# Kernel tuning notes

Hardware: AMD Instinct MI355X
Metric: run time of the kernel (lower is better)

The kernel has to match this reference:

```python
import jax, jax.numpy as jnp
import numpy as np

LEAK = 0.01  # torch LeakyReLU default negative_slope

def lrelu(x):
    return jnp.where(x >= 0, x, LEAK * x)

def edge_conv(x, src, dst, ea, W1, b1, W2, b2):
    # message: cat(x_i=target, x_j=source, edge_attr) -> Linear -> LeakyReLU -> Linear
    m = jnp.concatenate([x[dst], x[src], ea], axis=1)          # [E, 2F+Fe]
    h = lrelu(m @ W1 + b1) @ W2 + b2                            # [E, H]
    n = x.shape[0]
    agg = jnp.full((n, h.shape[1]), jnp.inf, h.dtype).at[dst].min(h)  # scatter-min at target
    return jnp.where(jnp.isfinite(agg), agg, jnp.zeros_like(agg))     # empty nodes -> 0


def setup_inputs() -> dict:
    key = jax.random.key(0)
    ks = jax.random.split(key, 20)
    B, N, E = 4, 20000, 640000
    NF, AD, EF, H = 2, 1, 1, 8
    inp = {
        "node_features": jax.random.randint(ks[0], (B, N, NF), 0, 10, dtype=jnp.int32),
        "actions": jax.random.normal(ks[1], (B, N), dtype=jnp.float32),
        "edge_index": jax.random.randint(ks[2], (B, 2, E), 0, N, dtype=jnp.int64),
        "edge_features": jax.random.normal(ks[3], (B, E, EF), dtype=jnp.float32),
    }
    d0 = NF + AD  # 3
    def lin(k, fin, fout):
        s = 1.0 / np.sqrt(fin)
        k1, k2 = jax.random.split(k)
        return (jax.random.uniform(k1, (fin, fout), jnp.float32, -s, s),
                jax.random.uniform(k2, (fout,), jnp.float32, -s, s))
    inp["c1_W1"], inp["c1_b1"] = lin(ks[4], 2 * d0 + EF, H)
    inp["c1_W2"], inp["c1_b2"] = lin(ks[5], H, H)
    inp["c2_W1"], inp["c2_b1"] = lin(ks[6], 2 * H + 1, H)
    inp["c2_W2"], inp["c2_b2"] = lin(ks[7], H, H)
    inp["c3_W1"], inp["c3_b1"] = lin(ks[8], 2 * H + 1, H)
    inp["c3_W2"], inp["c3_b2"] = lin(ks[9], H, H)
    inp["lin_W"], inp["lin_b"] = lin(ks[10], d0 + H, 1)
    return inp


def reference(node_features, actions, edge_index, edge_features,
              c1_W1, c1_b1, c1_W2, c1_b2,
              c2_W1, c2_b1, c2_W2, c2_b2,
              c3_W1, c3_b1, c3_W2, c3_b2,
              lin_W, lin_b):
    # x = int(node_features) concat actions  -> float
    x0 = jnp.concatenate([node_features.astype(jnp.int32).astype(jnp.float32),
                          actions[..., None]], axis=-1)  # [B,N,3]

    def per_graph(x0g, eig, eag):
        src, dst = eig[0], eig[1]  # flow source_to_target: x_j=src, x_i=dst
        h = lrelu(edge_conv(x0g, src, dst, eag, c1_W1, c1_b1, c1_W2, c1_b2))
        h = lrelu(edge_conv(h, src, dst, eag, c2_W1, c2_b1, c2_W2, c2_b2))
        h = lrelu(edge_conv(h, src, dst, eag, c3_W1, c3_b1, c3_W2, c3_b2))
        xc = jnp.concatenate([x0g, h], axis=1)  # [N, 3+8]
        return jnp.sum(xc, axis=0)              # sum-pool over nodes

    pooled = jax.vmap(per_graph)(x0, edge_index, edge_features)  # [B, 11]
    return pooled @ lin_W + lin_b  # [B, 1]
```

## Files before the change

### kernel.cpp

```cpp
#include <hip/hip_runtime.h>

#define LEAK 0.01f
#define BS 128
#define PCHUNK 8192
#define MAXTB 2048

__device__ __forceinline__ float lrelu(float v) {
    return v >= 0.f ? v : LEAK * v;
}

__device__ __forceinline__ unsigned int fmin_encode(float x) {
    unsigned int u = __float_as_uint(x);
    return (u & 0x80000000u) ? ~u : (u | 0x80000000u);
}
__device__ __forceinline__ float fmin_decode(unsigned int k) {
    unsigned int u = (k & 0x80000000u) ? (k ^ 0x80000000u) : ~k;
    return __uint_as_float(u);
}


__global__ __launch_bounds__(256) void node_init_kernel(
    const int* __restrict__ nf, const float* __restrict__ act,
    float* __restrict__ x0, int BN) {
    int tid = blockIdx.x * blockDim.x + threadIdx.x;
    if (tid >= BN) return;
    x0[tid * 3 + 0] = (float)nf[tid * 2 + 0];
    x0[tid * 3 + 1] = (float)nf[tid * 2 + 1];
    x0[tid * 3 + 2] = act[tid];
}

__global__ __launch_bounds__(256) void pool_kernel(
    const float* __restrict__ x0, const float* __restrict__ h,
    const float* __restrict__ lw, const float* __restrict__ lb,
    float* __restrict__ out, int N) {
    int b = blockIdx.y;
    int n = blockIdx.x * blockDim.x + threadIdx.x;
    float c = 0.f;
    if (n < N) {
        const float* x = x0 + ((size_t)b * N + n) * 3;
        const float* hh = h + ((size_t)b * N + n) * 8;
        c = x[0] * lw[0] + x[1] * lw[1] + x[2] * lw[2];
#pragma unroll
        for (int k = 0; k < 8; ++k) c = fmaf(hh[k], lw[3 + k], c);
    }
#pragma unroll
    for (int off = 32; off > 0; off >>= 1) c += __shfl_down(c, off, 64);
    __shared__ float wsum[4];
    int lane = threadIdx.x & 63;
    int wave = threadIdx.x >> 6;
    if (lane == 0) wsum[wave] = c;
    __syncthreads();
    if (threadIdx.x == 0) {
        float s = wsum[0] + wsum[1] + wsum[2] + wsum[3];
        if (blockIdx.x == 0) s += lb[0];
        atomicAdd(&out[b], s);
    }
}

template <int D>
__global__ __launch_bounds__(256) void precompute_kernel(
    const float* __restrict__ x, const float* __restrict__ W1,
    const float* __restrict__ b1, float* __restrict__ a1,
    float* __restrict__ a2, int BN) {
    int i = blockIdx.x * blockDim.x + threadIdx.x;
    if (i >= BN) return;
    float xi[D];
#pragma unroll
    for (int k = 0; k < D; ++k) xi[k] = x[(size_t)i * D + k];
    float v1[8], v2[8];
#pragma unroll
    for (int j = 0; j < 8; ++j) { v1[j] = b1[j]; v2[j] = 0.f; }
#pragma unroll
    for (int k = 0; k < D; ++k) {
        float xk = xi[k];
#pragma unroll
        for (int j = 0; j < 8; ++j) {
            v1[j] = fmaf(xk, W1[k * 8 + j], v1[j]);
            v2[j] = fmaf(xk, W1[(D + k) * 8 + j], v2[j]);
        }
    }
    float4* o1 = (float4*)(a1 + (size_t)i * 8);
    float4* o2 = (float4*)(a2 + (size_t)i * 8);
    o1[0] = make_float4(v1[0], v1[1], v1[2], v1[3]);
    o1[1] = make_float4(v1[4], v1[5], v1[6], v1[7]);
    o2[0] = make_float4(v2[0], v2[1], v2[2], v2[3]);
    o2[1] = make_float4(v2[4], v2[5], v2[6], v2[7]);
}


__global__ __launch_bounds__(256) void bucket_hist_kernel(
    const int* __restrict__ ei, int* __restrict__ bcnt,
    int E, int NB, int TB, int BE) {
    __shared__ int lc[MAXTB];
    int t = threadIdx.x;
    for (int i = t; i < TB; i += 256) lc[i] = 0;
    __syncthreads();
    int start = blockIdx.x * PCHUNK;
    int end = min(start + PCHUNK, BE);
    for (int e = start + t; e < end; e += 256) {
        int b = e / E;
        int idx = e - b * E;
        int d = ei[(size_t)b * 2 * E + E + idx];
        atomicAdd(&lc[b * NB + (d >> 7)], 1);
    }
    __syncthreads();
    for (int i = t; i < TB; i += 256)
        if (lc[i]) atomicAdd(&bcnt[i], lc[i]);
}

__global__ __launch_bounds__(1024) void bucket_scan_kernel(
    const int* __restrict__ bcnt, int* __restrict__ base,
    int* __restrict__ fill, int TB) {
    __shared__ int ts[1024];
    int t = threadIdx.x;
    int i0 = 2 * t, i1 = 2 * t + 1;
    int v0 = (i0 < TB) ? bcnt[i0] : 0;
    int v1 = (i1 < TB) ? bcnt[i1] : 0;
    int s = v0 + v1;
    ts[t] = s;
    __syncthreads();
    int incl = s;
    for (int off = 1; off < 1024; off <<= 1) {
        int add = (t >= off) ? ts[t - off] : 0;
        __syncthreads();
        incl += add;
        ts[t] = incl;
        __syncthreads();
    }
    int ex = incl - s;
    if (i0 < TB) { base[i0] = ex; fill[i0] = ex; }
    if (i1 < TB) { base[i1] = ex + v0; fill[i1] = ex + v0; }
    if (t == 0) base[TB] = ts[1023];
}

__global__ __launch_bounds__(256) void part_kernel(
    const int* __restrict__ ei, const float* __restrict__ ea,
    int* __restrict__ fill, int2* __restrict__ pairs,
    int E, int NB, int TB, int BE) {
    __shared__ int lc[MAXTB];
    __shared__ int lbase[MAXTB];
    int t = threadIdx.x;
    for (int i = t; i < TB; i += 256) lc[i] = 0;
    __syncthreads();
    int start = blockIdx.x * PCHUNK;
    int pk[32];
    for (int j = 0; j < 32; ++j) {
        int e = start + j * 256 + t;
        int p = -1;
        if (e < BE) {
            int b = e / E;
            int idx = e - b * E;
            int d = ei[(size_t)b * 2 * E + E + idx];
            int bkt = b * NB + (d >> 7);
            int r = atomicAdd(&lc[bkt], 1);
            p = bkt | (r << 12);
        }
        pk[j] = p;
    }
    __syncthreads();
    for (int i = t; i < TB; i += 256) {
        int c = lc[i];
        lbase[i] = c ? atomicAdd(&fill[i], c) : 0;
    }
    __syncthreads();
    for (int j = 0; j < 32; ++j) {
        int e = start + j * 256 + t;
        if (e < BE) {
            int b = e / E;
            int idx = e - b * E;
            const int* eb = ei + (size_t)b * 2 * E;
            int s = eb[idx];
            int d = eb[E + idx];
            int bkt = pk[j] & 0xFFF;
            int r = pk[j] >> 12;
            int pos = lbase[bkt] + r;
            pairs[pos] = make_int2(s | ((d & 127) << 16), __float_as_int(ea[e]));
        }
    }
}


__global__ __launch_bounds__(256) void conv_bucket_kernel(
    const float* __restrict__ a1, const float* __restrict__ a2,
    const float* __restrict__ w1e, const float* __restrict__ W2,
    const float* __restrict__ b2, const int* __restrict__ base,
    const int2* __restrict__ pairs, float* __restrict__ hout,
    int N, int NB) {
    __shared__ float a1s[BS * 9];
    __shared__ unsigned int acc[BS * 9];
    int bkt = blockIdx.x;
    int b = bkt / NB;
    int n0 = (bkt - b * NB) << 7;
    int nCnt = min(BS, N - n0);
    int t = threadIdx.x;
    size_t gn0 = ((size_t)b * N + n0) * 8;

    for (int i = t; i < nCnt * 8; i += 256)
        a1s[(i >> 3) * 9 + (i & 7)] = a1[gn0 + i];
    for (int i = t; i < BS * 9; i += 256) acc[i] = 0xFFFFFFFFu;

    float we[8], bb[8];
#pragma unroll
    for (int j = 0; j < 8; ++j) { we[j] = w1e[j]; bb[j] = b2[j]; }
    __syncthreads();

    int k1 = base[bkt + 1];
    size_t a2base = (size_t)b * N * 8;
    for (int k = base[bkt] + t; k < k1; k += 256) {
        int2 p = pairs[k];
        int s = p.x & 0xFFFF;
        int dl = (p.x >> 16) & 127;
        float eav = __int_as_float(p.y);
        const float4* a2p = (const float4*)(a2 + a2base + (size_t)s * 8);
        float4 lo = a2p[0], hi = a2p[1];
        float h1[8];
        h1[0] = a1s[dl * 9 + 0] + lo.x; h1[1] = a1s[dl * 9 + 1] + lo.y;
        h1[2] = a1s[dl * 9 + 2] + lo.z; h1[3] = a1s[dl * 9 + 3] + lo.w;
        h1[4] = a1s[dl * 9 + 4] + hi.x; h1[5] = a1s[dl * 9 + 5] + hi.y;
        h1[6] = a1s[dl * 9 + 6] + hi.z; h1[7] = a1s[dl * 9 + 7] + hi.w;
#pragma unroll
        for (int j = 0; j < 8; ++j) {
            h1[j] = fmaf(eav, we[j], h1[j]);
            h1[j] = lrelu(h1[j]);
        }
        float h2[8];
#pragma unroll
        for (int j = 0; j < 8; ++j) h2[j] = bb[j];
#pragma unroll
        for (int kk = 0; kk < 8; ++kk) {
            float hk = h1[kk];
#pragma unroll
            for (int j = 0; j < 8; ++j) h2[j] = fmaf(hk, W2[kk * 8 + j], h2[j]);
        }
#pragma unroll
        for (int j = 0; j < 8; ++j)
            atomicMin(&acc[dl * 9 + j], fmin_encode(h2[j]));
    }
    __syncthreads();

    for (int i = t; i < nCnt * 8; i += 256) {
        float v = fmin_decode(acc[(i >> 3) * 9 + (i & 7)]);
        unsigned int u = __float_as_uint(v);
        if ((u & 0x7F800000u) == 0x7F800000u) v = 0.f;
        hout[gn0 + i] = lrelu(v);
    }
}


template <int D>
__global__ __launch_bounds__(256) void edge_conv_kernel(
    const float* __restrict__ x, const int* __restrict__ ei,
    const float* __restrict__ ea,
    const float* __restrict__ W1, const float* __restrict__ b1,
    const float* __restrict__ W2, const float* __restrict__ b2,
    unsigned int* __restrict__ agg, int E, int N, int B) {
    int tid = blockIdx.x * blockDim.x + threadIdx.x;
    if (tid >= B * E) return;
    int b = tid / E;
    int e = tid - b * E;
    const int* eb = ei + (size_t)b * 2 * E;
    int s = eb[e];
    int d = eb[E + e];
    const float* xi = x + ((size_t)b * N + d) * D;
    const float* xj = x + ((size_t)b * N + s) * D;
    constexpr int M = 2 * D + 1;
    float m[M];
#pragma unroll
    for (int k = 0; k < D; ++k) { m[k] = xi[k]; m[D + k] = xj[k]; }
    m[2 * D] = ea[(size_t)b * E + e];
    float h1[8];
#pragma unroll
    for (int j = 0; j < 8; ++j) h1[j] = b1[j];
#pragma unroll
    for (int k = 0; k < M; ++k) {
        float mk = m[k];
#pragma unroll
        for (int j = 0; j < 8; ++j) h1[j] = fmaf(mk, W1[k * 8 + j], h1[j]);
    }
#pragma unroll
    for (int j = 0; j < 8; ++j) h1[j] = lrelu(h1[j]);
    float h2[8];
#pragma unroll
    for (int j = 0; j < 8; ++j) h2[j] = b2[j];
#pragma unroll
    for (int k = 0; k < 8; ++k) {
        float hk = h1[k];
#pragma unroll
        for (int j = 0; j < 8; ++j) h2[j] = fmaf(hk, W2[k * 8 + j], h2[j]);
    }
    unsigned int* ag = agg + ((size_t)b * N + d) * 8;
#pragma unroll
    for (int j = 0; j < 8; ++j) atomicMin(&ag[j], fmin_encode(h2[j]));
}

__global__ __launch_bounds__(256) void finalize_kernel(
    unsigned int* __restrict__ agg, int total) {
    int tid = blockIdx.x * blockDim.x + threadIdx.x;
    if (tid >= total) return;
    float v = fmin_decode(agg[tid]);
    unsigned int u = __float_as_uint(v);
    if ((u & 0x7F800000u) == 0x7F800000u) v = 0.f;
    ((float*)agg)[tid] = lrelu(v);
}


static inline size_t align256(size_t x) { return (x + 255) & ~(size_t)255; }

extern "C" void kernel_launch(void* const* d_in, const int* in_sizes, int n_in,
                              void* d_out, int out_size, void* d_ws, size_t ws_size,
                              hipStream_t stream) {
    const int B = 4;
    const int N = in_sizes[1] / B;
    const int E = in_sizes[2] / (2 * B);

    const int*   nf  = (const int*)d_in[0];
    const float* act = (const float*)d_in[1];
    const int*   ei  = (const int*)d_in[2];
    const float* ea  = (const float*)d_in[3];
    const float* c1_W1 = (const float*)d_in[4];
    const float* c1_b1 = (const float*)d_in[5];
    const float* c1_W2 = (const float*)d_in[6];
    const float* c1_b2 = (const float*)d_in[7];
    const float* c2_W1 = (const float*)d_in[8];
    const float* c2_b1 = (const float*)d_in[9];
    const float* c2_W2 = (const float*)d_in[10];
    const float* c2_b2 = (const float*)d_in[11];
    const float* c3_W1 = (const float*)d_in[12];
    const float* c3_b1 = (const float*)d_in[13];
    const float* c3_W2 = (const float*)d_in[14];
    const float* c3_b2 = (const float*)d_in[15];
    const float* lw    = (const float*)d_in[16];
    const float* lb    = (const float*)d_in[17];
    float* out = (float*)d_out;

    const int BN = B * N;
    const int BE = B * E;
    const int NB = (N + BS - 1) / BS;
    const int TB = B * NB;

    char* ws = (char*)d_ws;
    size_t off = 0;
    float* x0   = (float*)(ws + off);  off += align256((size_t)BN * 3 * 4);
    float* bufA = (float*)(ws + off);  off += align256((size_t)BN * 8 * 4);
    float* bufB = (float*)(ws + off);  off += align256((size_t)BN * 8 * 4);
    float* a1   = (float*)(ws + off);  off += align256((size_t)BN * 8 * 4);
    float* a2   = (float*)(ws + off);  off += align256((size_t)BN * 8 * 4);
    int* bcnt   = (int*)(ws + off);    off += align256((size_t)TB * 4);
    int* base   = (int*)(ws + off);    off += align256((size_t)(TB + 1) * 4);
    int* fill   = (int*)(ws + off);    off += align256((size_t)TB * 4);
    int2* pairs = (int2*)(ws + off);   off += align256((size_t)BE * 8);
    const bool useFast = (off <= ws_size) && (TB <= MAXTB) && (N <= 65536);

    hipMemsetAsync(out, 0, (size_t)B * sizeof(float), stream);
    node_init_kernel<<<(BN + 255) / 256, 256, 0, stream>>>(nf, act, x0, BN);

    const int ngrid = (BN + 255) / 256;
    const int pgrid1 = (BE + PCHUNK - 1) / PCHUNK;

    if (useFast) {
        hipMemsetAsync(bcnt, 0, (size_t)TB * 4, stream);
        bucket_hist_kernel<<<pgrid1, 256, 0, stream>>>(ei, bcnt, E, NB, TB, BE);
        bucket_scan_kernel<<<1, 1024, 0, stream>>>(bcnt, base, fill, TB);
        part_kernel<<<pgrid1, 256, 0, stream>>>(ei, ea, fill, pairs, E, NB, TB, BE);

        precompute_kernel<3><<<ngrid, 256, 0, stream>>>(x0, c1_W1, c1_b1, a1, a2, BN);
        conv_bucket_kernel<<<TB, 256, 0, stream>>>(a1, a2, c1_W1 + 6 * 8, c1_W2, c1_b2,
                                                   base, pairs, bufA, N, NB);
        precompute_kernel<8><<<ngrid, 256, 0, stream>>>(bufA, c2_W1, c2_b1, a1, a2, BN);
        conv_bucket_kernel<<<TB, 256, 0, stream>>>(a1, a2, c2_W1 + 16 * 8, c2_W2, c2_b2,
                                                   base, pairs, bufB, N, NB);
        precompute_kernel<8><<<ngrid, 256, 0, stream>>>(bufB, c3_W1, c3_b1, a1, a2, BN);
        conv_bucket_kernel<<<TB, 256, 0, stream>>>(a1, a2, c3_W1 + 16 * 8, c3_W2, c3_b2,
                                                   base, pairs, bufA, N, NB);
    } else {
        const int egrid = (BE + 255) / 256;
        const int aggTotal = BN * 8;
        const int agrid = (aggTotal + 255) / 256;
        const size_t aggBytes = (size_t)aggTotal * 4;
        unsigned int* uA = (unsigned int*)bufA;
        unsigned int* uB = (unsigned int*)bufB;

        hipMemsetAsync(uA, 0xFF, aggBytes, stream);
        edge_conv_kernel<3><<<egrid, 256, 0, stream>>>(
            x0, ei, ea, c1_W1, c1_b1, c1_W2, c1_b2, uA, E, N, B);
        finalize_kernel<<<agrid, 256, 0, stream>>>(uA, aggTotal);

        hipMemsetAsync(uB, 0xFF, aggBytes, stream);
        edge_conv_kernel<8><<<egrid, 256, 0, stream>>>(
            (const float*)uA, ei, ea, c2_W1, c2_b1, c2_W2, c2_b2, uB, E, N, B);
        finalize_kernel<<<agrid, 256, 0, stream>>>(uB, aggTotal);

        hipMemsetAsync(uA, 0xFF, aggBytes, stream);
        edge_conv_kernel<8><<<egrid, 256, 0, stream>>>(
            (const float*)uB, ei, ea, c3_W1, c3_b1, c3_W2, c3_b2, uA, E, N, B);
        finalize_kernel<<<agrid, 256, 0, stream>>>(uA, aggTotal);
    }

    dim3 pgrid((N + 255) / 256, B);
    pool_kernel<<<pgrid, 256, 0, stream>>>(x0, (const float*)bufA, lw, lb, out, N);
}
```

Measured before the change: 247.1 us.

## Fuse node init, next-layer precompute and pooling into bucketed conv kernels

The fast path now does node init, first-layer precompute and the x0 part of pooling in one kernel. Each conv layer's epilogue computes the next layer's a1/a2 projections from shared memory, and the last conv pools directly into the output. This removes the separate precompute, pool and init launches along with their global round-trips. It also partitions edges per graph with a 2D grid and smaller chunks, avoiding the per-edge division, and processes two edges per thread iteration to raise memory-level parallelism. The cost is more work in the conv epilogues and a larger partition grid with more global atomics.

```diff
diff --git a/kernel.cpp b/kernel.cpp
--- a/kernel.cpp
+++ b/kernel.cpp
@@ -2,8 +2,8 @@
 
 #define LEAK 0.01f
 #define BS 128
-#define PCHUNK 8192
-#define MAXTB 2048
+#define PCHUNK 2048
+#define MAXNB 1024
 
 __device__ __forceinline__ float lrelu(float v) {
     return v >= 0.f ? v : LEAK * v;
@@ -16,6 +16,285 @@
 __device__ __forceinline__ float fmin_decode(unsigned int k) {
     unsigned int u = (k & 0x80000000u) ? (k ^ 0x80000000u) : ~k;
     return __uint_as_float(u);
+}
+
+__device__ __forceinline__ void block_add(float c, float* dst) {
+    __shared__ float wsum[4];
+#pragma unroll
+    for (int off = 32; off > 0; off >>= 1) c += __shfl_down(c, off, 64);
+    int lane = threadIdx.x & 63;
+    int wave = threadIdx.x >> 6;
+    if (lane == 0) wsum[wave] = c;
+    __syncthreads();
+    if (threadIdx.x == 0)
+        atomicAdd(dst, wsum[0] + wsum[1] + wsum[2] + wsum[3]);
+}
+
+__global__ __launch_bounds__(256) void init_pre1_kernel(
+    const int* __restrict__ nf, const float* __restrict__ act,
+    const float* __restrict__ W1, const float* __restrict__ b1,
+    const float* __restrict__ lw, const float* __restrict__ lb,
+    float* __restrict__ a1, float* __restrict__ a2,
+    float* __restrict__ out, int N) {
+    int b = blockIdx.y;
+    int n = blockIdx.x * 256 + threadIdx.x;
+    float c = 0.f;
+    if (n < N) {
+        size_t i = (size_t)b * N + n;
+        float x0 = (float)nf[i * 2 + 0];
+        float x1 = (float)nf[i * 2 + 1];
+        float x2 = act[i];
+        float v1[8], v2[8];
+#pragma unroll
+        for (int j = 0; j < 8; ++j) {
+            v1[j] = b1[j] + x0 * W1[0 * 8 + j] + x1 * W1[1 * 8 + j] + x2 * W1[2 * 8 + j];
+            v2[j] =         x0 * W1[3 * 8 + j] + x1 * W1[4 * 8 + j] + x2 * W1[5 * 8 + j];
+        }
+        float4* o1 = (float4*)(a1 + i * 8);
+        float4* o2 = (float4*)(a2 + i * 8);
+        o1[0] = make_float4(v1[0], v1[1], v1[2], v1[3]);
+        o1[1] = make_float4(v1[4], v1[5], v1[6], v1[7]);
+        o2[0] = make_float4(v2[0], v2[1], v2[2], v2[3]);
+        o2[1] = make_float4(v2[4], v2[5], v2[6], v2[7]);
+        c = x0 * lw[0] + x1 * lw[1] + x2 * lw[2];
+        if (n == 0) c += lb[0];
+    }
+    block_add(c, &out[b]);
+}
+
+
+__global__ __launch_bounds__(256) void bucket_hist_kernel(
+    const int* __restrict__ ei, int* __restrict__ bcnt, int E, int NB) {
+    __shared__ int lc[MAXNB];
+    int b = blockIdx.y;
+    int t = threadIdx.x;
+    for (int i = t; i < NB; i += 256) lc[i] = 0;
+    __syncthreads();
+    int e0 = blockIdx.x * PCHUNK;
+    int end = min(e0 + PCHUNK, E);
+    const int* drow = ei + (size_t)b * 2 * E + E;
+    for (int e = e0 + t; e < end; e += 256)
+        atomicAdd(&lc[drow[e] >> 7], 1);
+    __syncthreads();
+    for (int i = t; i < NB; i += 256)
+        if (lc[i]) atomicAdd(&bcnt[b * NB + i], lc[i]);
+}
+
+__global__ __launch_bounds__(1024) void bucket_scan_kernel(
+    const int* __restrict__ bcnt, int* __restrict__ base,
+    int* __restrict__ fill, int TB) {
+    __shared__ int ts[1024];
+    int t = threadIdx.x;
+    int i0 = 2 * t, i1 = 2 * t + 1;
+    int v0 = (i0 < TB) ? bcnt[i0] : 0;
+    int v1 = (i1 < TB) ? bcnt[i1] : 0;
+    int s = v0 + v1;
+    ts[t] = s;
+    __syncthreads();
+    int incl = s;
+    for (int off = 1; off < 1024; off <<= 1) {
+        int add = (t >= off) ? ts[t - off] : 0;
+        __syncthreads();
+        incl += add;
+        ts[t] = incl;
+        __syncthreads();
+    }
+    int ex = incl - s;
+    if (i0 < TB) { base[i0] = ex; fill[i0] = ex; }
+    if (i1 < TB) { base[i1] = ex + v0; fill[i1] = ex + v0; }
+    if (t == 0) base[TB] = ts[1023];
+}
+
+__global__ __launch_bounds__(256) void part_kernel(
+    const int* __restrict__ ei, const float* __restrict__ ea,
+    int* __restrict__ fill, int2* __restrict__ pairs, int E, int NB) {
+    __shared__ int lc[MAXNB];
+    __shared__ int lbase[MAXNB];
+    int b = blockIdx.y;
+    int t = threadIdx.x;
+    for (int i = t; i < NB; i += 256) lc[i] = 0;
+    __syncthreads();
+    int e0 = blockIdx.x * PCHUNK;
+    int end = min(e0 + PCHUNK, E);
+    const int* srow = ei + (size_t)b * 2 * E;
+    const int* drow = srow + E;
+    int pk[PCHUNK / 256];
+#pragma unroll
+    for (int j = 0; j < PCHUNK / 256; ++j) {
+        int e = e0 + j * 256 + t;
+        int p = -1;
+        if (e < end) {
+            int d = drow[e];
+            int bin = d >> 7;
+            int r = atomicAdd(&lc[bin], 1);
+            p = bin | ((d & 127) << 10) | (r << 17);
+        }
+        pk[j] = p;
+    }
+    __syncthreads();
+    for (int i = t; i < NB; i += 256) {
+        int c = lc[i];
+        lbase[i] = c ? atomicAdd(&fill[b * NB + i], c) : 0;
+    }
+    __syncthreads();
+#pragma unroll
+    for (int j = 0; j < PCHUNK / 256; ++j) {
+        int e = e0 + j * 256 + t;
+        if (e < end) {
+            int p = pk[j];
+            int bin = p & 1023;
+            int dl = (p >> 10) & 127;
+            int r = p >> 17;
+            pairs[lbase[bin] + r] =
+                make_int2(srow[e] | (dl << 16), __float_as_int(ea[(size_t)b * E + e]));
+        }
+    }
+}
+
+
+__device__ __forceinline__ void conv_edges(
+    const float* __restrict__ a2g, const float* we, const float* bb,
+    const float* __restrict__ W2, const int2* __restrict__ pairs,
+    int k0, int k1, const float* __restrict__ a1s, unsigned int* __restrict__ acc) {
+    int t = threadIdx.x;
+    for (int k = k0 + t; k < k1; k += 512) {
+        int2 p0 = pairs[k];
+        bool has1 = (k + 256 < k1);
+        int2 p1 = has1 ? pairs[k + 256] : p0;
+        const float4* q0 = (const float4*)(a2g + (size_t)(p0.x & 0xFFFF) * 8);
+        float4 lo0 = q0[0], hi0 = q0[1];
+        const float4* q1 = (const float4*)(a2g + (size_t)(p1.x & 0xFFFF) * 8);
+        float4 lo1 = q1[0], hi1 = q1[1];
+#pragma unroll
+        for (int which = 0; which < 2; ++which) {
+            if (which == 1 && !has1) break;
+            int dl = ((which ? p1.x : p0.x) >> 16) & 127;
+            float eav = __int_as_float(which ? p1.y : p0.y);
+            float4 lo = which ? lo1 : lo0;
+            float4 hi = which ? hi1 : hi0;
+            float h1[8];
+            h1[0] = a1s[dl * 9 + 0] + lo.x; h1[1] = a1s[dl * 9 + 1] + lo.y;
+            h1[2] = a1s[dl * 9 + 2] + lo.z; h1[3] = a1s[dl * 9 + 3] + lo.w;
+            h1[4] = a1s[dl * 9 + 4] + hi.x; h1[5] = a1s[dl * 9 + 5] + hi.y;
+            h1[6] = a1s[dl * 9 + 6] + hi.z; h1[7] = a1s[dl * 9 + 7] + hi.w;
+#pragma unroll
+            for (int j = 0; j < 8; ++j) {
+                h1[j] = fmaf(eav, we[j], h1[j]);
+                h1[j] = lrelu(h1[j]);
+            }
+            float h2[8];
+#pragma unroll
+            for (int j = 0; j < 8; ++j) h2[j] = bb[j];
+#pragma unroll
+            for (int kk = 0; kk < 8; ++kk) {
+                float hk = h1[kk];
+#pragma unroll
+                for (int j = 0; j < 8; ++j) h2[j] = fmaf(hk, W2[kk * 8 + j], h2[j]);
+            }
+#pragma unroll
+            for (int j = 0; j < 8; ++j)
+                atomicMin(&acc[dl * 9 + j], fmin_encode(h2[j]));
+        }
+    }
+}
+
+__global__ __launch_bounds__(256) void conv_mid_kernel(
+    const float* __restrict__ a1, const float* __restrict__ a2,
+    const float* __restrict__ w1e, const float* __restrict__ W2,
+    const float* __restrict__ b2,
+    const float* __restrict__ nW1, const float* __restrict__ nb1,
+    const int* __restrict__ base, const int2* __restrict__ pairs,
+    float* __restrict__ na1, float* __restrict__ na2, int N, int NB) {
+    __shared__ float a1s[BS * 9];
+    __shared__ unsigned int acc[BS * 9];
+    int b = blockIdx.y;
+    int bkt = b * NB + blockIdx.x;
+    int n0 = blockIdx.x << 7;
+    int nCnt = min(BS, N - n0);
+    int t = threadIdx.x;
+    size_t gn0 = ((size_t)b * N + n0) * 8;
+
+    for (int i = t; i < nCnt * 8; i += 256)
+        a1s[(i >> 3) * 9 + (i & 7)] = a1[gn0 + i];
+    for (int i = t; i < BS * 9; i += 256) acc[i] = 0xFFFFFFFFu;
+    float we[8], bb[8];
+#pragma unroll
+    for (int j = 0; j < 8; ++j) { we[j] = w1e[j]; bb[j] = b2[j]; }
+    __syncthreads();
+
+    conv_edges(a2 + (size_t)b * N * 8, we, bb, W2, pairs, base[bkt], base[bkt + 1],
+               a1s, acc);
+    __syncthreads();
+
+    for (int i = t; i < nCnt * 8; i += 256) {
+        float v = fmin_decode(acc[(i >> 3) * 9 + (i & 7)]);
+        unsigned int u = __float_as_uint(v);
+        if ((u & 0x7F800000u) == 0x7F800000u) v = 0.f;
+        a1s[(i >> 3) * 9 + (i & 7)] = lrelu(v);
+    }
+    __syncthreads();
+
+    int node = t >> 1, half = t & 1;
+    if (node < nCnt) {
+        float h[8];
+#pragma unroll
+        for (int j = 0; j < 8; ++j) h[j] = a1s[node * 9 + j];
+        float v[8];
+#pragma unroll
+        for (int j = 0; j < 8; ++j) v[j] = half ? 0.f : nb1[j];
+        const float* Wbase = nW1 + (half ? 64 : 0);
+#pragma unroll
+        for (int k = 0; k < 8; ++k) {
+            float hk = h[k];
+#pragma unroll
+            for (int j = 0; j < 8; ++j) v[j] = fmaf(hk, Wbase[k * 8 + j], v[j]);
+        }
+        float* dst = (half ? na2 : na1) + gn0 + (size_t)node * 8;
+        float4* o = (float4*)dst;
+        o[0] = make_float4(v[0], v[1], v[2], v[3]);
+        o[1] = make_float4(v[4], v[5], v[6], v[7]);
+    }
+}
+
+__global__ __launch_bounds__(256) void conv_final_kernel(
+    const float* __restrict__ a1, const float* __restrict__ a2,
+    const float* __restrict__ w1e, const float* __restrict__ W2,
+    const float* __restrict__ b2, const float* __restrict__ lw,
+    const int* __restrict__ base, const int2* __restrict__ pairs,
+    float* __restrict__ out, int N, int NB) {
+    __shared__ float a1s[BS * 9];
+    __shared__ unsigned int acc[BS * 9];
+    int b = blockIdx.y;
+    int bkt = b * NB + blockIdx.x;
+    int n0 = blockIdx.x << 7;
+    int nCnt = min(BS, N - n0);
+    int t = threadIdx.x;
+    size_t gn0 = ((size_t)b * N + n0) * 8;
+
+    for (int i = t; i < nCnt * 8; i += 256)
+        a1s[(i >> 3) * 9 + (i & 7)] = a1[gn0 + i];
+    for (int i = t; i < BS * 9; i += 256) acc[i] = 0xFFFFFFFFu;
+    float we[8], bb[8];
+#pragma unroll
+    for (int j = 0; j < 8; ++j) { we[j] = w1e[j]; bb[j] = b2[j]; }
+    __syncthreads();
+
+    conv_edges(a2 + (size_t)b * N * 8, we, bb, W2, pairs, base[bkt], base[bkt + 1],
+               a1s, acc);
+    __syncthreads();
+
+    float c = 0.f;
+    if (t < nCnt) {
+#pragma unroll
+        for (int j = 0; j < 8; ++j) {
+            float v = fmin_decode(acc[t * 9 + j]);
+            unsigned int u = __float_as_uint(v);
+            if ((u & 0x7F800000u) == 0x7F800000u) v = 0.f;
+            c = fmaf(lrelu(v), lw[3 + j], c);
+        }
+    }
+    __syncthreads();
+    block_add(c, &out[b]);
 }
 
 
@@ -28,224 +307,6 @@
     x0[tid * 3 + 1] = (float)nf[tid * 2 + 1];
     x0[tid * 3 + 2] = act[tid];
 }
-
-__global__ __launch_bounds__(256) void pool_kernel(
-    const float* __restrict__ x0, const float* __restrict__ h,
-    const float* __restrict__ lw, const float* __restrict__ lb,
-    float* __restrict__ out, int N) {
-    int b = blockIdx.y;
-    int n = blockIdx.x * blockDim.x + threadIdx.x;
-    float c = 0.f;
-    if (n < N) {
-        const float* x = x0 + ((size_t)b * N + n) * 3;
-        const float* hh = h + ((size_t)b * N + n) * 8;
-        c = x[0] * lw[0] + x[1] * lw[1] + x[2] * lw[2];
-#pragma unroll
-        for (int k = 0; k < 8; ++k) c = fmaf(hh[k], lw[3 + k], c);
-    }
-#pragma unroll
-    for (int off = 32; off > 0; off >>= 1) c += __shfl_down(c, off, 64);
-    __shared__ float wsum[4];
-    int lane = threadIdx.x & 63;
-    int wave = threadIdx.x >> 6;
-    if (lane == 0) wsum[wave] = c;
-    __syncthreads();
-    if (threadIdx.x == 0) {
-        float s = wsum[0] + wsum[1] + wsum[2] + wsum[3];
-        if (blockIdx.x == 0) s += lb[0];
-        atomicAdd(&out[b], s);
-    }
-}
-
-template <int D>
-__global__ __launch_bounds__(256) void precompute_kernel(
-    const float* __restrict__ x, const float* __restrict__ W1,
-    const float* __restrict__ b1, float* __restrict__ a1,
-    float* __restrict__ a2, int BN) {
-    int i = blockIdx.x * blockDim.x + threadIdx.x;
-    if (i >= BN) return;
-    float xi[D];
-#pragma unroll
-    for (int k = 0; k < D; ++k) xi[k] = x[(size_t)i * D + k];
-    float v1[8], v2[8];
-#pragma unroll
-    for (int j = 0; j < 8; ++j) { v1[j] = b1[j]; v2[j] = 0.f; }
-#pragma unroll
-    for (int k = 0; k < D; ++k) {
-        float xk = xi[k];
-#pragma unroll
-        for (int j = 0; j < 8; ++j) {
-            v1[j] = fmaf(xk, W1[k * 8 + j], v1[j]);
-            v2[j] = fmaf(xk, W1[(D + k) * 8 + j], v2[j]);
-        }
-    }
-    float4* o1 = (float4*)(a1 + (size_t)i * 8);
-    float4* o2 = (float4*)(a2 + (size_t)i * 8);
-    o1[0] = make_float4(v1[0], v1[1], v1[2], v1[3]);
-    o1[1] = make_float4(v1[4], v1[5], v1[6], v1[7]);
-    o2[0] = make_float4(v2[0], v2[1], v2[2], v2[3]);
-    o2[1] = make_float4(v2[4], v2[5], v2[6], v2[7]);
-}
-
-
-__global__ __launch_bounds__(256) void bucket_hist_kernel(
-    const int* __restrict__ ei, int* __restrict__ bcnt,
-    int E, int NB, int TB, int BE) {
-    __shared__ int lc[MAXTB];
-    int t = threadIdx.x;
-    for (int i = t; i < TB; i += 256) lc[i] = 0;
-    __syncthreads();
-    int start = blockIdx.x * PCHUNK;
-    int end = min(start + PCHUNK, BE);
-    for (int e = start + t; e < end; e += 256) {
-        int b = e / E;
-        int idx = e - b * E;
-        int d = ei[(size_t)b * 2 * E + E + idx];
-        atomicAdd(&lc[b * NB + (d >> 7)], 1);
-    }
-    __syncthreads();
-    for (int i = t; i < TB; i += 256)
-        if (lc[i]) atomicAdd(&bcnt[i], lc[i]);
-}
-
-__global__ __launch_bounds__(1024) void bucket_scan_kernel(
-    const int* __restrict__ bcnt, int* __restrict__ base,
-    int* __restrict__ fill, int TB) {
-    __shared__ int ts[1024];
-    int t = threadIdx.x;
-    int i0 = 2 * t, i1 = 2 * t + 1;
-    int v0 = (i0 < TB) ? bcnt[i0] : 0;
-    int v1 = (i1 < TB) ? bcnt[i1] : 0;
-    int s = v0 + v1;
-    ts[t] = s;
-    __syncthreads();
-    int incl = s;
-    for (int off = 1; off < 1024; off <<= 1) {
-        int add = (t >= off) ? ts[t - off] : 0;
-        __syncthreads();
-        incl += add;
-        ts[t] = incl;
-        __syncthreads();
-    }
-    int ex = incl - s;
-    if (i0 < TB) { base[i0] = ex; fill[i0] = ex; }
-    if (i1 < TB) { base[i1] = ex + v0; fill[i1] = ex + v0; }
-    if (t == 0) base[TB] = ts[1023];
-}
-
-__global__ __launch_bounds__(256) void part_kernel(
-    const int* __restrict__ ei, const float* __restrict__ ea,
-    int* __restrict__ fill, int2* __restrict__ pairs,
-    int E, int NB, int TB, int BE) {
-    __shared__ int lc[MAXTB];
-    __shared__ int lbase[MAXTB];
-    int t = threadIdx.x;
-    for (int i = t; i < TB; i += 256) lc[i] = 0;
-    __syncthreads();
-    int start = blockIdx.x * PCHUNK;
-    int pk[32];
-    for (int j = 0; j < 32; ++j) {
-        int e = start + j * 256 + t;
-        int p = -1;
-        if (e < BE) {
-            int b = e / E;
-            int idx = e - b * E;
-            int d = ei[(size_t)b * 2 * E + E + idx];
-            int bkt = b * NB + (d >> 7);
-            int r = atomicAdd(&lc[bkt], 1);
-            p = bkt | (r << 12);
-        }
-        pk[j] = p;
-    }
-    __syncthreads();
-    for (int i = t; i < TB; i += 256) {
-        int c = lc[i];
-        lbase[i] = c ? atomicAdd(&fill[i], c) : 0;
-    }
-    __syncthreads();
-    for (int j = 0; j < 32; ++j) {
-        int e = start + j * 256 + t;
-        if (e < BE) {
-            int b = e / E;
-            int idx = e - b * E;
-            const int* eb = ei + (size_t)b * 2 * E;
-            int s = eb[idx];
-            int d = eb[E + idx];
-            int bkt = pk[j] & 0xFFF;
-            int r = pk[j] >> 12;
-            int pos = lbase[bkt] + r;
-            pairs[pos] = make_int2(s | ((d & 127) << 16), __float_as_int(ea[e]));
-        }
-    }
-}
-
-
-__global__ __launch_bounds__(256) void conv_bucket_kernel(
-    const float* __restrict__ a1, const float* __restrict__ a2,
-    const float* __restrict__ w1e, const float* __restrict__ W2,
-    const float* __restrict__ b2, const int* __restrict__ base,
-    const int2* __restrict__ pairs, float* __restrict__ hout,
-    int N, int NB) {
-    __shared__ float a1s[BS * 9];
-    __shared__ unsigned int acc[BS * 9];
-    int bkt = blockIdx.x;
-    int b = bkt / NB;
-    int n0 = (bkt - b * NB) << 7;
-    int nCnt = min(BS, N - n0);
-    int t = threadIdx.x;
-    size_t gn0 = ((size_t)b * N + n0) * 8;
-
-    for (int i = t; i < nCnt * 8; i += 256)
-        a1s[(i >> 3) * 9 + (i & 7)] = a1[gn0 + i];
-    for (int i = t; i < BS * 9; i += 256) acc[i] = 0xFFFFFFFFu;
-
-    float we[8], bb[8];
-#pragma unroll
-    for (int j = 0; j < 8; ++j) { we[j] = w1e[j]; bb[j] = b2[j]; }
-    __syncthreads();
-
-    int k1 = base[bkt + 1];
-    size_t a2base = (size_t)b * N * 8;
-    for (int k = base[bkt] + t; k < k1; k += 256) {
-        int2 p = pairs[k];
-        int s = p.x & 0xFFFF;
-        int dl = (p.x >> 16) & 127;
-        float eav = __int_as_float(p.y);
-        const float4* a2p = (const float4*)(a2 + a2base + (size_t)s * 8);
-        float4 lo = a2p[0], hi = a2p[1];
-        float h1[8];
-        h1[0] = a1s[dl * 9 + 0] + lo.x; h1[1] = a1s[dl * 9 + 1] + lo.y;
-        h1[2] = a1s[dl * 9 + 2] + lo.z; h1[3] = a1s[dl * 9 + 3] + lo.w;
-        h1[4] = a1s[dl * 9 + 4] + hi.x; h1[5] = a1s[dl * 9 + 5] + hi.y;
-        h1[6] = a1s[dl * 9 + 6] + hi.z; h1[7] = a1s[dl * 9 + 7] + hi.w;
-#pragma unroll
-        for (int j = 0; j < 8; ++j) {
-            h1[j] = fmaf(eav, we[j], h1[j]);
-            h1[j] = lrelu(h1[j]);
-        }
-        float h2[8];
-#pragma unroll
-        for (int j = 0; j < 8; ++j) h2[j] = bb[j];
-#pragma unroll
-        for (int kk = 0; kk < 8; ++kk) {
-            float hk = h1[kk];
-#pragma unroll
-            for (int j = 0; j < 8; ++j) h2[j] = fmaf(hk, W2[kk * 8 + j], h2[j]);
-        }
-#pragma unroll
-        for (int j = 0; j < 8; ++j)
-            atomicMin(&acc[dl * 9 + j], fmin_encode(h2[j]));
-    }
-    __syncthreads();
-
-    for (int i = t; i < nCnt * 8; i += 256) {
-        float v = fmin_decode(acc[(i >> 3) * 9 + (i & 7)]);
-        unsigned int u = __float_as_uint(v);
-        if ((u & 0x7F800000u) == 0x7F800000u) v = 0.f;
-        hout[gn0 + i] = lrelu(v);
-    }
-}
-
 
 template <int D>
 __global__ __launch_bounds__(256) void edge_conv_kernel(
@@ -301,6 +362,24 @@
     unsigned int u = __float_as_uint(v);
     if ((u & 0x7F800000u) == 0x7F800000u) v = 0.f;
     ((float*)agg)[tid] = lrelu(v);
+}
+
+__global__ __launch_bounds__(256) void pool_kernel(
+    const float* __restrict__ x0, const float* __restrict__ h,
+    const float* __restrict__ lw, const float* __restrict__ lb,
+    float* __restrict__ out, int N) {
+    int b = blockIdx.y;
+    int n = blockIdx.x * blockDim.x + threadIdx.x;
+    float c = 0.f;
+    if (n < N) {
+        const float* x = x0 + ((size_t)b * N + n) * 3;
+        const float* hh = h + ((size_t)b * N + n) * 8;
+        c = x[0] * lw[0] + x[1] * lw[1] + x[2] * lw[2];
+#pragma unroll
+        for (int k = 0; k < 8; ++k) c = fmaf(hh[k], lw[3 + k], c);
+        if (n == 0) c += lb[0];
+    }
+    block_add(c, &out[b]);
 }
 
 
@@ -337,48 +416,54 @@
     const int BE = B * E;
     const int NB = (N + BS - 1) / BS;
     const int TB = B * NB;
+    const int CPG = (E + PCHUNK - 1) / PCHUNK;
 
     char* ws = (char*)d_ws;
     size_t off = 0;
-    float* x0   = (float*)(ws + off);  off += align256((size_t)BN * 3 * 4);
-    float* bufA = (float*)(ws + off);  off += align256((size_t)BN * 8 * 4);
-    float* bufB = (float*)(ws + off);  off += align256((size_t)BN * 8 * 4);
-    float* a1   = (float*)(ws + off);  off += align256((size_t)BN * 8 * 4);
-    float* a2   = (float*)(ws + off);  off += align256((size_t)BN * 8 * 4);
+    float* a1A  = (float*)(ws + off);  off += align256((size_t)BN * 8 * 4);
+    float* a2A  = (float*)(ws + off);  off += align256((size_t)BN * 8 * 4);
+    float* a1B  = (float*)(ws + off);  off += align256((size_t)BN * 8 * 4);
+    float* a2B  = (float*)(ws + off);  off += align256((size_t)BN * 8 * 4);
     int* bcnt   = (int*)(ws + off);    off += align256((size_t)TB * 4);
     int* base   = (int*)(ws + off);    off += align256((size_t)(TB + 1) * 4);
     int* fill   = (int*)(ws + off);    off += align256((size_t)TB * 4);
     int2* pairs = (int2*)(ws + off);   off += align256((size_t)BE * 8);
-    const bool useFast = (off <= ws_size) && (TB <= MAXTB) && (N <= 65536);
+    float* x0   = (float*)(ws + off);  off += align256((size_t)BN * 3 * 4);
+    const bool useFast = (off <= ws_size) && (NB <= MAXNB) && (TB <= 2048) &&
+                         (N <= 65536);
 
     hipMemsetAsync(out, 0, (size_t)B * sizeof(float), stream);
-    node_init_kernel<<<(BN + 255) / 256, 256, 0, stream>>>(nf, act, x0, BN);
-
-    const int ngrid = (BN + 255) / 256;
-    const int pgrid1 = (BE + PCHUNK - 1) / PCHUNK;
 
     if (useFast) {
+        dim3 egrid(CPG, B);
+        dim3 igrid((N + 255) / 256, B);
+        dim3 cgrid(NB, B);
+
         hipMemsetAsync(bcnt, 0, (size_t)TB * 4, stream);
-        bucket_hist_kernel<<<pgrid1, 256, 0, stream>>>(ei, bcnt, E, NB, TB, BE);
+        init_pre1_kernel<<<igrid, 256, 0, stream>>>(nf, act, c1_W1, c1_b1,
+                                                    lw, lb, a1A, a2A, out, N);
+        bucket_hist_kernel<<<egrid, 256, 0, stream>>>(ei, bcnt, E, NB);
         bucket_scan_kernel<<<1, 1024, 0, stream>>>(bcnt, base, fill, TB);
-        part_kernel<<<pgrid1, 256, 0, stream>>>(ei, ea, fill, pairs, E, NB, TB, BE);
-
-        precompute_kernel<3><<<ngrid, 256, 0, stream>>>(x0, c1_W1, c1_b1, a1, a2, BN);
-        conv_bucket_kernel<<<TB, 256, 0, stream>>>(a1, a2, c1_W1 + 6 * 8, c1_W2, c1_b2,
-                                                   base, pairs, bufA, N, NB);
-        precompute_kernel<8><<<ngrid, 256, 0, stream>>>(bufA, c2_W1, c2_b1, a1, a2, BN);
-        conv_bucket_kernel<<<TB, 256, 0, stream>>>(a1, a2, c2_W1 + 16 * 8, c2_W2, c2_b2,
-                                                   base, pairs, bufB, N, NB);
-        precompute_kernel<8><<<ngrid, 256, 0, stream>>>(bufB, c3_W1, c3_b1, a1, a2, BN);
-        conv_bucket_kernel<<<TB, 256, 0, stream>>>(a1, a2, c3_W1 + 16 * 8, c3_W2, c3_b2,
-                                                   base, pairs, bufA, N, NB);
+        part_kernel<<<egrid, 256, 0, stream>>>(ei, ea, fill, pairs, E, NB);
+
+        conv_mid_kernel<<<cgrid, 256, 0, stream>>>(
+            a1A, a2A, c1_W1 + 6 * 8, c1_W2, c1_b2, c2_W1, c2_b1,
+            base, pairs, a1B, a2B, N, NB);
+        conv_mid_kernel<<<cgrid, 256, 0, stream>>>(
+            a1B, a2B, c2_W1 + 16 * 8, c2_W2, c2_b2, c3_W1, c3_b1,
+            base, pairs, a1A, a2A, N, NB);
+        conv_final_kernel<<<cgrid, 256, 0, stream>>>(
+            a1A, a2A, c3_W1 + 16 * 8, c3_W2, c3_b2, lw,
+            base, pairs, out, N, NB);
     } else {
         const int egrid = (BE + 255) / 256;
         const int aggTotal = BN * 8;
         const int agrid = (aggTotal + 255) / 256;
         const size_t aggBytes = (size_t)aggTotal * 4;
-        unsigned int* uA = (unsigned int*)bufA;
-        unsigned int* uB = (unsigned int*)bufB;
+        unsigned int* uA = (unsigned int*)a1A;
+        unsigned int* uB = (unsigned int*)a1B;
+
+        node_init_kernel<<<(BN + 255) / 256, 256, 0, stream>>>(nf, act, x0, BN);
 
         hipMemsetAsync(uA, 0xFF, aggBytes, stream);
         edge_conv_kernel<3><<<egrid, 256, 0, stream>>>(
@@ -394,8 +479,8 @@
         edge_conv_kernel<8><<<egrid, 256, 0, stream>>>(
             (const float*)uB, ei, ea, c3_W1, c3_b1, c3_W2, c3_b2, uA, E, N, B);
         finalize_kernel<<<agrid, 256, 0, stream>>>(uA, aggTotal);
-    }
-
-    dim3 pgrid((N + 255) / 256, B);
-    pool_kernel<<<pgrid, 256, 0, stream>>>(x0, (const float*)bufA, lw, lb, out, N);
-}
+
+        dim3 pgrid((N + 255) / 256, B);
+        pool_kernel<<<pgrid, 256, 0, stream>>>(x0, (const float*)uA, lw, lb, out, N);
+    }
+}
```

New measurement: 235.4 us. 4.7% less time.
